# Optimization experiments

Hardware: AMD Instinct MI355X
Metric: run time of the kernel (lower is better)

The kernel has to match this reference:

```python
import jax, jax.numpy as jnp
import numpy as np

L, H, C, T, V = 6, 12, 768, 1024, 50257
HD = C // H
B = 2
EPS = 1e-5


def setup_inputs() -> dict:
    key = jax.random.key(0)
    ks = jax.random.split(key, 10)
    std = 0.02
    proj_std = 0.02 / np.sqrt(2 * L)  # specialized init for projection layers

    def n(k, shape, s=std):
        return jax.random.normal(k, shape, dtype=jnp.float32) * s

    return {
        "tokens": jax.random.randint(ks[0], (B, T), 0, V),
        "tok_emb": n(ks[1], (V, C)),
        "pos_emb": n(ks[2], (T, C)),
        # per-layer stacked params, leading dim L (scanned)
        "Wq": n(ks[3], (L, H, C, HD)),
        "Wk": n(ks[4], (L, H, C, HD)),
        "Wv": n(ks[5], (L, H, C, HD)),
        "Wo": n(ks[6], (L, C, C), proj_std),
        "bo": jnp.zeros((L, C), jnp.float32),
        "ln1_g": jnp.ones((L, C), jnp.float32),
        "ln1_b": jnp.zeros((L, C), jnp.float32),
        "ln2_g": jnp.ones((L, C), jnp.float32),
        "ln2_b": jnp.zeros((L, C), jnp.float32),
        "W1": n(ks[7], (L, C, 4 * C)),
        "b1": jnp.zeros((L, 4 * C), jnp.float32),
        "W2": n(ks[8], (L, 4 * C, C), proj_std),
        "b2": jnp.zeros((L, C), jnp.float32),
        "lnf_g": jnp.ones((C,), jnp.float32),
        "lnf_b": jnp.zeros((C,), jnp.float32),
        "head_w": n(ks[9], (C, V)),
        "head_b": jnp.zeros((V,), jnp.float32),
    }


def _ln(x, g, b):
    m = x.mean(-1, keepdims=True)
    v = ((x - m) ** 2).mean(-1, keepdims=True)
    return (x - m) * jax.lax.rsqrt(v + EPS) * g + b


def _forward(tokens, p):
    x = p["tok_emb"][tokens] + p["pos_emb"][None, : tokens.shape[1]]  # [B,T,C]
    mask = jnp.tril(jnp.ones((T, T), dtype=bool))
    scale = C ** -0.5  # NOTE: original scales by input channel C, not head_size

    def block(x, lp):
        Wq, Wk, Wv, Wo, bo, g1, b1, g2, b2, W1, bb1, W2, bb2 = lp
        # NOTE: original writes x = ln1(x); x = x + attn(x)  (residual from normed x)
        x = _ln(x, g1, b1)
        q = jnp.einsum("btc,hcd->bhtd", x, Wq)
        k = jnp.einsum("btc,hcd->bhtd", x, Wk)
        v = jnp.einsum("btc,hcd->bhtd", x, Wv)
        s = jnp.einsum("bhtd,bhsd->bhts", q, k) * scale
        s = jnp.where(mask, s, -jnp.inf)
        a = jax.nn.softmax(s, axis=-1)
        y = jnp.einsum("bhts,bhsd->bhtd", a, v)
        y = y.transpose(0, 2, 1, 3).reshape(x.shape)  # concat heads -> [B,T,C]
        x = x + y @ Wo + bo
        x = _ln(x, g2, b2)
        h = jax.nn.gelu(x @ W1 + bb1, approximate=False)  # torch GELU = exact erf
        x = x + h @ W2 + bb2
        return x, None

    lps = (p["Wq"], p["Wk"], p["Wv"], p["Wo"], p["bo"], p["ln1_g"], p["ln1_b"],
           p["ln2_g"], p["ln2_b"], p["W1"], p["b1"], p["W2"], p["b2"])
    x, _ = jax.lax.scan(block, x, lps)
    x = _ln(x, p["lnf_g"], p["lnf_b"])
    return x @ p["head_w"] + p["head_b"]  # [B,T,V]


def reference(tokens, tok_emb, pos_emb, Wq, Wk, Wv, Wo, bo, ln1_g, ln1_b,
              ln2_g, ln2_b, W1, b1, W2, b2, lnf_g, lnf_b, head_w, head_b):
    p = dict(tok_emb=tok_emb, pos_emb=pos_emb, Wq=Wq, Wk=Wk, Wv=Wv, Wo=Wo, bo=bo,
             ln1_g=ln1_g, ln1_b=ln1_b, ln2_g=ln2_g, ln2_b=ln2_b, W1=W1, b1=b1,
             W2=W2, b2=b2, lnf_g=lnf_g, lnf_b=lnf_b, head_w=head_w, head_b=head_b)
    return _forward(tokens, p)
```

## Files before the change

kernel.cpp:

```cpp
#include <hip/hip_runtime.h>
#include <hip/hip_bf16.h>
#include <stdint.h>
#include <math.h>


#define L_ 6
#define H_ 12
#define C_ 768
#define T_ 1024
#define V_ 50257
#define VP_ 50304
#define HD_ 64
#define BT_ 2048
#define F_ 3072
#define SCALE_ 0.03608439182435161f
#define NEGBIG_ -1e30f

typedef __bf16 bf;
typedef __attribute__((ext_vector_type(8))) __bf16 bf16x8;
typedef __attribute__((ext_vector_type(4))) __bf16 bf16x4;
typedef __attribute__((ext_vector_type(4))) float f32x4;

__device__ __forceinline__ void gload16(const void* g, void* l) {
  __builtin_amdgcn_global_load_lds(
      (const __attribute__((address_space(1))) unsigned int*)g,
      (__attribute__((address_space(3))) unsigned int*)l, 16, 0, 0);
}

__device__ __forceinline__ float gelu_f(float x) {
  return 0.5f * x * (1.0f + erff(x * 0.70710678118654752f));
}

__global__ __launch_bounds__(256) void embed_k(const int* __restrict__ tok,
                                               const float* __restrict__ te,
                                               const float* __restrict__ pe,
                                               float* __restrict__ x) {
  int bt = blockIdx.x;
  int c = blockIdx.y * 256 + threadIdx.x;
  int t = bt & (T_ - 1);
  int v = tok[bt];
  x[(size_t)bt * C_ + c] = te[(size_t)v * C_ + c] + pe[(size_t)t * C_ + c];
}

__global__ __launch_bounds__(256) void ln_k(const float* __restrict__ xin,
                                            float* __restrict__ xout,
                                            bf* __restrict__ xb,
                                            const float* __restrict__ g,
                                            const float* __restrict__ b) {
  int row = blockIdx.x;
  const float* xr = xin + (size_t)row * C_;
  int tid = threadIdx.x;
  float v0 = xr[tid], v1 = xr[tid + 256], v2 = xr[tid + 512];
  float s1 = v0 + v1 + v2;
  float s2 = v0 * v0 + v1 * v1 + v2 * v2;
#pragma unroll
  for (int o = 32; o > 0; o >>= 1) {
    s1 += __shfl_xor(s1, o, 64);
    s2 += __shfl_xor(s2, o, 64);
  }
  __shared__ float r1[4], r2[4];
  int w = tid >> 6, lane = tid & 63;
  if (lane == 0) { r1[w] = s1; r2[w] = s2; }
  __syncthreads();
  float S1 = r1[0] + r1[1] + r1[2] + r1[3];
  float S2 = r2[0] + r2[1] + r2[2] + r2[3];
  float mean = S1 * (1.0f / C_);
  float var = S2 * (1.0f / C_) - mean * mean;
  float rs = rsqrtf(fmaxf(var, 0.0f) + 1e-5f);
  float* xo = xout + (size_t)row * C_;
  bf* xbo = xb + (size_t)row * C_;
  float vv[3] = {v0, v1, v2};
#pragma unroll
  for (int j = 0; j < 3; ++j) {
    int c = tid + j * 256;
    float o = (vv[j] - mean) * rs * g[c] + b[c];
    xo[c] = o;
    xbo[c] = (bf)o;
  }
}

__device__ __forceinline__ void transpose_body(const float* __restrict__ src,
                                               bf* __restrict__ dst, int src_ld,
                                               int dst_ld, int k0, int n0,
                                               int nmax) {
  __shared__ __align__(16) bf tl[64][72];
  int tid = threadIdx.x;
  int r = tid >> 2;
  int cb = (tid & 3) * 16;
#pragma unroll
  for (int j4 = 0; j4 < 4; ++j4) {
    int c = cb + j4 * 4;
    int n = n0 + c;
    size_t idx = (size_t)(k0 + r) * src_ld + n;
    const float* sp = src + idx;
    if (n + 4 <= nmax && (idx & 3) == 0) {
      f32x4 v = *(const f32x4*)sp;
      tl[r][c] = (bf)v[0];
      tl[r][c + 1] = (bf)v[1];
      tl[r][c + 2] = (bf)v[2];
      tl[r][c + 3] = (bf)v[3];
    } else {
#pragma unroll
      for (int j = 0; j < 4; ++j)
        tl[r][c + j] = (n + j < nmax) ? (bf)sp[j] : (bf)0.0f;
    }
  }
  __syncthreads();
  int n = n0 + r;
  bf16x8 w0, w1;
#pragma unroll
  for (int j = 0; j < 8; ++j) {
    w0[j] = tl[cb + j][r];
    w1[j] = tl[cb + 8 + j][r];
  }
  bf* dp = dst + (size_t)n * dst_ld + k0 + cb;
  *(bf16x8*)dp = w0;
  *(bf16x8*)(dp + 8) = w1;
}

__global__ __launch_bounds__(256) void transpose_k(const float* __restrict__ src,
                                                   bf* __restrict__ dst,
                                                   int src_ld, int dst_ld,
                                                   int nmax) {
  transpose_body(src, dst, src_ld, dst_ld, blockIdx.x * 64, blockIdx.y * 64,
                 nmax);
}

__global__ __launch_bounds__(256) void trans_layer_k(
    const float* __restrict__ Wq, const float* __restrict__ Wk,
    const float* __restrict__ Wv, const float* __restrict__ Wo,
    const float* __restrict__ W1, const float* __restrict__ W2,
    bf* __restrict__ wqkvT, bf* __restrict__ woT, bf* __restrict__ w1T,
    bf* __restrict__ w2T) {
  int r = blockIdx.x;
  if (r < 432) {
    int z = r / 12, k0 = (r % 12) * 64;
    int tsel = z / H_, hh = z % H_;
    const float* W = (tsel == 0) ? Wq : (tsel == 1) ? Wk : Wv;
    transpose_body(W + (size_t)hh * C_ * HD_,
                   wqkvT + (size_t)(tsel * C_ + hh * HD_) * C_, HD_, C_, k0, 0,
                   HD_);
  } else if (r < 576) {
    r -= 432;
    transpose_body(Wo, woT, C_, C_, (r % 12) * 64, (r / 12) * 64, C_);
  } else if (r < 1152) {
    r -= 576;
    transpose_body(W1, w1T, F_, C_, (r % 12) * 64, (r / 12) * 64, F_);
  } else {
    r -= 1152;
    transpose_body(W2, w2T, C_, F_, (r % 48) * 64, (r / 48) * 64, C_);
  }
}

template <int MODE, int BM, int BN>
__global__ __launch_bounds__(256) void gemm_bt(const bf* __restrict__ A,
                                               const bf* __restrict__ Bt,
                                               const float* __restrict__ bias,
                                               float* __restrict__ xres,
                                               bf* __restrict__ o0,
                                               bf* __restrict__ o1,
                                               bf* __restrict__ o2, int K) {
  constexpr int WM = BM / 2, WN = BN / 2;
  constexpr int MI = WM / 16, NJ = WN / 16;
  __shared__ __align__(16) bf smem[(BM + BN) * 64];
  bf* aL = smem;
  bf* bL = smem + BM * 64;
  const int tid = threadIdx.x;
  const int w = tid >> 6, lane = tid & 63;
  const int wm = w >> 1, wn = w & 1;
  const int lm = lane & 15, lg = lane >> 4;

  const int lin = blockIdx.y * gridDim.x + blockIdx.x;
  const int q8 = (gridDim.x * gridDim.y) >> 3;
  const int wg = (lin & 7) * q8 + (lin >> 3);
  const int mt = gridDim.y;
  const int m0 = (wg % mt) * BM, n0 = (wg / mt) * BN;

  const int lr8 = lane >> 3;
  const int lc8s = ((lane & 7) ^ lr8) * 8;

  f32x4 acc[MI][NJ];
#pragma unroll
  for (int i = 0; i < MI; ++i)
#pragma unroll
    for (int j = 0; j < NJ; ++j) acc[i][j] = (f32x4){0.f, 0.f, 0.f, 0.f};

  const int cXor = (lm & 7) * 8;
  for (int k0 = 0; k0 < K; k0 += 64) {
#pragma unroll
    for (int c = 0; c < BM / 32; ++c) {
      int row = w * (BM / 4) + c * 8;
      gload16(A + (size_t)(m0 + row + lr8) * K + k0 + lc8s, &aL[row * 64]);
    }
#pragma unroll
    for (int c = 0; c < BN / 32; ++c) {
      int row = w * (BN / 4) + c * 8;
      gload16(Bt + (size_t)(n0 + row + lr8) * K + k0 + lc8s, &bL[row * 64]);
    }
    __syncthreads();
#pragma unroll
    for (int ks = 0; ks < 2; ++ks) {
      const int cc = (ks * 32 + lg * 8) ^ cXor;
      bf16x8 af[MI], bfv[NJ];
#pragma unroll
      for (int i = 0; i < MI; ++i)
        af[i] = *(const bf16x8*)&aL[(wm * WM + i * 16 + lm) * 64 + cc];
#pragma unroll
      for (int j = 0; j < NJ; ++j)
        bfv[j] = *(const bf16x8*)&bL[(wn * WN + j * 16 + lm) * 64 + cc];
#pragma unroll
      for (int i = 0; i < MI; ++i)
#pragma unroll
        for (int j = 0; j < NJ; ++j)
          acc[i][j] = __builtin_amdgcn_mfma_f32_16x16x32_bf16(
              af[i], bfv[j], acc[i][j], 0, 0, 0);
    }
    __syncthreads();
  }

  if constexpr (MODE == 3) {
    int ngj[NJ];
    float bv[NJ];
#pragma unroll
    for (int j = 0; j < NJ; ++j) {
      ngj[j] = n0 + wn * WN + j * 16 + lm;
      bv[j] = (ngj[j] < V_) ? bias[ngj[j]] : 0.f;
    }
#pragma unroll
    for (int i = 0; i < MI; ++i)
#pragma unroll
      for (int r = 0; r < 4; ++r) {
        int row = m0 + wm * WM + i * 16 + lg * 4 + r;
        float* orow = xres + (size_t)row * V_;
#pragma unroll
        for (int j = 0; j < NJ; ++j)
          if (ngj[j] < V_) orow[ngj[j]] = acc[i][j][r] + bv[j];
      }
    return;
  }

  if constexpr (MODE == 0) {
    const int bb = m0 >> 10;
    if (n0 >= 2 * C_) {
      bf* sv = smem;
      __syncthreads();
#pragma unroll
      for (int i = 0; i < MI; ++i)
#pragma unroll
        for (int j = 0; j < NJ; ++j) {
          int dl = wn * WN + j * 16 + lm;
#pragma unroll
          for (int r = 0; r < 4; ++r) {
            int tl = wm * WM + i * 16 + lg * 4 + r;
            sv[dl * (BM + 8) + tl] = (bf)acc[i][j][r];
          }
        }
      __syncthreads();
      int dd_l = tid >> 1, half = tid & 1;
      size_t vrow = (size_t)bb * C_ + (n0 - 2 * C_) + dd_l;
      int t_base = m0 & (T_ - 1);
#pragma unroll
      for (int s = 0; s < 4; ++s) {
        int tt = half * 32 + s * 8;
        *(bf16x8*)(o2 + vrow * T_ + t_base + tt) =
            *(const bf16x8*)&sv[dd_l * (BM + 8) + tt];
      }
      return;
    }
    bf* dst = (n0 < C_) ? o0 : o1;
    int nb = (n0 < C_) ? n0 : n0 - C_;
    size_t basej[NJ];
#pragma unroll
    for (int j = 0; j < NJ; ++j) {
      int rr = nb + wn * WN + j * 16 + lm;
      int hh = rr >> 6, dd = rr & 63;
      basej[j] = ((size_t)(bb * H_ + hh) * T_) * HD_ + dd;
    }
#pragma unroll
    for (int i = 0; i < MI; ++i)
#pragma unroll
      for (int r = 0; r < 4; ++r) {
        int tt = (m0 + wm * WM + i * 16 + lg * 4 + r) & (T_ - 1);
#pragma unroll
        for (int j = 0; j < NJ; ++j)
          dst[basej[j] + (size_t)tt * HD_] = (bf)acc[i][j][r];
      }
    return;
  }

  int ngj[NJ];
  float bv[NJ];
#pragma unroll
  for (int j = 0; j < NJ; ++j) {
    ngj[j] = n0 + wn * WN + j * 16 + lm;
    bv[j] = bias[ngj[j]];
  }
#pragma unroll
  for (int i = 0; i < MI; ++i)
#pragma unroll
    for (int r = 0; r < 4; ++r) {
      int row = m0 + wm * WM + i * 16 + lg * 4 + r;
      if constexpr (MODE == 1) {
        float* xrow = xres + (size_t)row * C_;
#pragma unroll
        for (int j = 0; j < NJ; ++j) xrow[ngj[j]] += acc[i][j][r] + bv[j];
      } else {
        bf* orow = o0 + (size_t)row * F_;
#pragma unroll
        for (int j = 0; j < NJ; ++j)
          orow[ngj[j]] = (bf)gelu_f(acc[i][j][r] + bv[j]);
      }
    }
}

__global__ __launch_bounds__(256) void attn_k(const bf* __restrict__ q,
                                              const bf* __restrict__ k,
                                              const bf* __restrict__ vt,
                                              bf* __restrict__ yb) {
  const int qb = blockIdx.x, bh = blockIdx.y;
  const int tid = threadIdx.x, w = tid >> 6, lane = tid & 63;
  const int lm = lane & 15, lg = lane >> 4;
  const int bb = bh / H_, hh = bh % H_;
  __shared__ __align__(16) bf kl[64 * 64];
  __shared__ __align__(16) bf vl[64 * 64];
  __shared__ __align__(16) bf pl[4][16 * 64];

  const int qrow = qb * 64 + w * 16 + lm;
  const bf* qbase = q + ((size_t)bh * T_ + qrow) * HD_;
  bf16x8 qf0 = *(const bf16x8*)(qbase + lg * 8);
  bf16x8 qf1 = *(const bf16x8*)(qbase + 32 + lg * 8);

  f32x4 y[4];
#pragma unroll
  for (int i = 0; i < 4; ++i) y[i] = (f32x4){0.f, 0.f, 0.f, 0.f};
  float m_run = NEGBIG_, l_run = 0.f;

  for (int kb = 0; kb <= qb; ++kb) {
#pragma unroll
    for (int c = 0; c < 2; ++c) {
      int rbase = w * 16 + c * 8;
      gload16(k + ((size_t)bh * T_ + kb * 64 + rbase + lane / 8) * HD_ +
                  (lane % 8) * 8,
              &kl[rbase * 64]);
      gload16(vt + ((size_t)bh * HD_ + rbase + lane / 8) * T_ + kb * 64 +
                  (lane % 8) * 8,
              &vl[rbase * 64]);
    }
    __syncthreads();

    f32x4 s[4];
#pragma unroll
    for (int t = 0; t < 4; ++t) {
      s[t] = (f32x4){0.f, 0.f, 0.f, 0.f};
      bf16x8 a0 = *(const bf16x8*)&kl[(t * 16 + lm) * 64 + lg * 8];
      s[t] = __builtin_amdgcn_mfma_f32_16x16x32_bf16(a0, qf0, s[t], 0, 0, 0);
      bf16x8 a1 = *(const bf16x8*)&kl[(t * 16 + lm) * 64 + 32 + lg * 8];
      s[t] = __builtin_amdgcn_mfma_f32_16x16x32_bf16(a1, qf1, s[t], 0, 0, 0);
    }

    float mx = NEGBIG_;
#pragma unroll
    for (int t = 0; t < 4; ++t)
#pragma unroll
      for (int r = 0; r < 4; ++r) {
        float v = s[t][r] * SCALE_;
        int kv = kb * 64 + t * 16 + lg * 4 + r;
        if (kb == qb && kv > qrow) v = NEGBIG_;
        s[t][r] = v;
        mx = fmaxf(mx, v);
      }
    mx = fmaxf(mx, __shfl_xor(mx, 16, 64));
    mx = fmaxf(mx, __shfl_xor(mx, 32, 64));
    float mnew = fmaxf(m_run, mx);
    float corr = __expf(m_run - mnew);
    float rs = 0.f;
#pragma unroll
    for (int t = 0; t < 4; ++t)
#pragma unroll
      for (int r = 0; r < 4; ++r) {
        float p = __expf(s[t][r] - mnew);
        s[t][r] = p;
        rs += p;
      }
    rs += __shfl_xor(rs, 16, 64);
    rs += __shfl_xor(rs, 32, 64);
    l_run = l_run * corr + rs;
    m_run = mnew;

#pragma unroll
    for (int t = 0; t < 4; ++t) {
      bf16x4 pk;
#pragma unroll
      for (int r = 0; r < 4; ++r) pk[r] = (bf)s[t][r];
      *(bf16x4*)&pl[w][lm * 64 + t * 16 + lg * 4] = pk;
    }

    float cy0 = __shfl(corr, lg * 4 + 0, 64);
    float cy1 = __shfl(corr, lg * 4 + 1, 64);
    float cy2 = __shfl(corr, lg * 4 + 2, 64);
    float cy3 = __shfl(corr, lg * 4 + 3, 64);
#pragma unroll
    for (int nt = 0; nt < 4; ++nt) {
      y[nt][0] *= cy0;
      y[nt][1] *= cy1;
      y[nt][2] *= cy2;
      y[nt][3] *= cy3;
    }

#pragma unroll
    for (int nt = 0; nt < 4; ++nt)
#pragma unroll
      for (int ks = 0; ks < 2; ++ks) {
        bf16x8 ap = *(const bf16x8*)&pl[w][lm * 64 + ks * 32 + lg * 8];
        bf16x8 bv = *(const bf16x8*)&vl[(nt * 16 + lm) * 64 + ks * 32 + lg * 8];
        y[nt] = __builtin_amdgcn_mfma_f32_16x16x32_bf16(ap, bv, y[nt], 0, 0, 0);
      }
    __syncthreads();
  }

  float ly[4];
#pragma unroll
  for (int r = 0; r < 4; ++r) ly[r] = __shfl(l_run, lg * 4 + r, 64);
#pragma unroll
  for (int nt = 0; nt < 4; ++nt) {
    int cc = hh * 64 + nt * 16 + lm;
#pragma unroll
    for (int r = 0; r < 4; ++r) {
      int qr = qb * 64 + w * 16 + lg * 4 + r;
      yb[((size_t)(bb * T_ + qr)) * C_ + cc] = (bf)(y[nt][r] / ly[r]);
    }
  }
}

extern "C" void kernel_launch(void* const* d_in, const int* in_sizes, int n_in,
                              void* d_out, int out_size, void* d_ws,
                              size_t ws_size, hipStream_t stream) {
  (void)in_sizes; (void)n_in; (void)out_size; (void)ws_size;
  const int* tokens = (const int*)d_in[0];
  const float* tok_emb = (const float*)d_in[1];
  const float* pos_emb = (const float*)d_in[2];
  const float* Wq = (const float*)d_in[3];
  const float* Wk = (const float*)d_in[4];
  const float* Wv = (const float*)d_in[5];
  const float* Wo = (const float*)d_in[6];
  const float* bo = (const float*)d_in[7];
  const float* ln1g = (const float*)d_in[8];
  const float* ln1b = (const float*)d_in[9];
  const float* ln2g = (const float*)d_in[10];
  const float* ln2b = (const float*)d_in[11];
  const float* W1 = (const float*)d_in[12];
  const float* b1 = (const float*)d_in[13];
  const float* W2 = (const float*)d_in[14];
  const float* b2 = (const float*)d_in[15];
  const float* lnfg = (const float*)d_in[16];
  const float* lnfb = (const float*)d_in[17];
  const float* headw = (const float*)d_in[18];
  const float* headb = (const float*)d_in[19];
  float* out = (float*)d_out;

  uint8_t* base = (uint8_t*)d_ws;
  size_t off = 0;
  auto alloc = [&](size_t n) -> uint8_t* {
    uint8_t* r = base + off;
    off += (n + 255) & ~(size_t)255;
    return r;
  };
  float* x = (float*)alloc((size_t)BT_ * C_ * 4);
  bf* xb = (bf*)alloc((size_t)BT_ * C_ * 2);
  bf* qq = (bf*)alloc((size_t)BT_ * C_ * 2);
  bf* kk = (bf*)alloc((size_t)BT_ * C_ * 2);
  bf* vt = (bf*)alloc((size_t)BT_ * C_ * 2);
  bf* ybuf = (bf*)alloc((size_t)BT_ * C_ * 2);
  bf* hb = (bf*)alloc((size_t)BT_ * F_ * 2);
  bf* wqkvT = (bf*)alloc((size_t)3 * C_ * C_ * 2);
  bf* woT = (bf*)alloc((size_t)C_ * C_ * 2);
  bf* w1T = (bf*)alloc((size_t)F_ * C_ * 2);
  bf* w2T = (bf*)alloc((size_t)C_ * F_ * 2);
  bf* headT = (bf*)alloc((size_t)VP_ * C_ * 2);

  dim3 blk(256);
  transpose_k<<<dim3(C_ / 64, VP_ / 64), blk, 0, stream>>>(headw, headT, V_,
                                                           C_, V_);
  embed_k<<<dim3(BT_, 3), blk, 0, stream>>>(tokens, tok_emb, pos_emb, x);

  for (int l = 0; l < L_; ++l) {
    trans_layer_k<<<1728, blk, 0, stream>>>(
        Wq + (size_t)l * H_ * C_ * HD_, Wk + (size_t)l * H_ * C_ * HD_,
        Wv + (size_t)l * H_ * C_ * HD_, Wo + (size_t)l * C_ * C_,
        W1 + (size_t)l * C_ * F_, W2 + (size_t)l * F_ * C_, wqkvT, woT, w1T,
        w2T);

    ln_k<<<BT_, blk, 0, stream>>>(x, x, xb, ln1g + l * C_, ln1b + l * C_);
    gemm_bt<0, 64, 128><<<dim3(2304 / 128, BT_ / 64), blk, 0, stream>>>(
        xb, wqkvT, nullptr, nullptr, qq, kk, vt, C_);
    attn_k<<<dim3(T_ / 64, 2 * H_), blk, 0, stream>>>(qq, kk, vt, ybuf);
    gemm_bt<1, 64, 64><<<dim3(C_ / 64, BT_ / 64), blk, 0, stream>>>(
        ybuf, woT, bo + l * C_, x, nullptr, nullptr, nullptr, C_);
    ln_k<<<BT_, blk, 0, stream>>>(x, x, xb, ln2g + l * C_, ln2b + l * C_);
    gemm_bt<2, 128, 128><<<dim3(F_ / 128, BT_ / 128), blk, 0, stream>>>(
        xb, w1T, b1 + l * F_, nullptr, hb, nullptr, nullptr, C_);
    gemm_bt<1, 64, 64><<<dim3(C_ / 64, BT_ / 64), blk, 0, stream>>>(
        hb, w2T, b2 + l * C_, x, nullptr, nullptr, nullptr, F_);
  }

  ln_k<<<BT_, blk, 0, stream>>>(x, x, xb, lnfg, lnfb);
  gemm_bt<3, 128, 128><<<dim3(VP_ / 128, BT_ / 128), blk, 0, stream>>>(
      xb, headT, headb, out, nullptr, nullptr, nullptr, C_);
}
```

Baseline: 1.374 ms.

## Double-buffer LDS tiles in GEMM and attention to overlap loads with MFMA

```diff
diff --git a/kernel.cpp b/kernel.cpp
--- a/kernel.cpp
+++ b/kernel.cpp
@@ -162,9 +162,8 @@
                                                bf* __restrict__ o2, int K) {
   constexpr int WM = BM / 2, WN = BN / 2;
   constexpr int MI = WM / 16, NJ = WN / 16;
-  __shared__ __align__(16) bf smem[(BM + BN) * 64];
-  bf* aL = smem;
-  bf* bL = smem + BM * 64;
+  constexpr int HALF = (BM + BN) * 64;
+  __shared__ __align__(16) bf smem[2 * HALF];
   const int tid = threadIdx.x;
   const int w = tid >> 6, lane = tid & 63;
   const int wm = w >> 1, wn = w & 1;
@@ -179,14 +178,9 @@
   const int lr8 = lane >> 3;
   const int lc8s = ((lane & 7) ^ lr8) * 8;
 
-  f32x4 acc[MI][NJ];
-#pragma unroll
-  for (int i = 0; i < MI; ++i)
-#pragma unroll
-    for (int j = 0; j < NJ; ++j) acc[i][j] = (f32x4){0.f, 0.f, 0.f, 0.f};
-
-  const int cXor = (lm & 7) * 8;
-  for (int k0 = 0; k0 < K; k0 += 64) {
+  auto stage = [&](int buf, int k0) {
+    bf* aL = smem + buf * HALF;
+    bf* bL = aL + BM * 64;
 #pragma unroll
     for (int c = 0; c < BM / 32; ++c) {
       int row = w * (BM / 4) + c * 8;
@@ -197,7 +191,23 @@
       int row = w * (BN / 4) + c * 8;
       gload16(Bt + (size_t)(n0 + row + lr8) * K + k0 + lc8s, &bL[row * 64]);
     }
-    __syncthreads();
+  };
+
+  f32x4 acc[MI][NJ];
+#pragma unroll
+  for (int i = 0; i < MI; ++i)
+#pragma unroll
+    for (int j = 0; j < NJ; ++j) acc[i][j] = (f32x4){0.f, 0.f, 0.f, 0.f};
+
+  const int cXor = (lm & 7) * 8;
+  const int NT = K >> 6;
+  stage(0, 0);
+  __syncthreads();
+  int cur = 0;
+  for (int t = 0; t < NT; ++t) {
+    if (t + 1 < NT) stage(cur ^ 1, (t + 1) << 6);
+    const bf* aL = smem + cur * HALF;
+    const bf* bL = aL + BM * 64;
 #pragma unroll
     for (int ks = 0; ks < 2; ++ks) {
       const int cc = (ks * 32 + lg * 8) ^ cXor;
@@ -216,6 +226,7 @@
               af[i], bfv[j], acc[i][j], 0, 0, 0);
     }
     __syncthreads();
+    cur ^= 1;
   }
 
   if constexpr (MODE == 3) {
@@ -243,7 +254,6 @@
     const int bb = m0 >> 10;
     if (n0 >= 2 * C_) {
       bf* sv = smem;
-      __syncthreads();
 #pragma unroll
       for (int i = 0; i < MI; ++i)
 #pragma unroll
@@ -321,9 +331,22 @@
   const int tid = threadIdx.x, w = tid >> 6, lane = tid & 63;
   const int lm = lane & 15, lg = lane >> 4;
   const int bb = bh / H_, hh = bh % H_;
-  __shared__ __align__(16) bf kl[64 * 64];
-  __shared__ __align__(16) bf vl[64 * 64];
+  __shared__ __align__(16) bf kl[2][64 * 64];
+  __shared__ __align__(16) bf vl[2][64 * 64];
   __shared__ __align__(16) bf pl[4][16 * 64];
+
+  auto stage = [&](int buf, int kb) {
+#pragma unroll
+    for (int c = 0; c < 2; ++c) {
+      int rbase = w * 16 + c * 8;
+      gload16(k + ((size_t)bh * T_ + kb * 64 + rbase + lane / 8) * HD_ +
+                  (lane % 8) * 8,
+              &kl[buf][rbase * 64]);
+      gload16(vt + ((size_t)bh * HD_ + rbase + lane / 8) * T_ + kb * 64 +
+                  (lane % 8) * 8,
+              &vl[buf][rbase * 64]);
+    }
+  };
 
   const int qrow = qb * 64 + w * 16 + lm;
   const bf* qbase = q + ((size_t)bh * T_ + qrow) * HD_;
@@ -335,26 +358,19 @@
   for (int i = 0; i < 4; ++i) y[i] = (f32x4){0.f, 0.f, 0.f, 0.f};
   float m_run = NEGBIG_, l_run = 0.f;
 
+  stage(0, 0);
+  __syncthreads();
+  int cur = 0;
   for (int kb = 0; kb <= qb; ++kb) {
-#pragma unroll
-    for (int c = 0; c < 2; ++c) {
-      int rbase = w * 16 + c * 8;
-      gload16(k + ((size_t)bh * T_ + kb * 64 + rbase + lane / 8) * HD_ +
-                  (lane % 8) * 8,
-              &kl[rbase * 64]);
-      gload16(vt + ((size_t)bh * HD_ + rbase + lane / 8) * T_ + kb * 64 +
-                  (lane % 8) * 8,
-              &vl[rbase * 64]);
-    }
-    __syncthreads();
+    if (kb < qb) stage(cur ^ 1, kb + 1);
 
     f32x4 s[4];
 #pragma unroll
     for (int t = 0; t < 4; ++t) {
       s[t] = (f32x4){0.f, 0.f, 0.f, 0.f};
-      bf16x8 a0 = *(const bf16x8*)&kl[(t * 16 + lm) * 64 + lg * 8];
+      bf16x8 a0 = *(const bf16x8*)&kl[cur][(t * 16 + lm) * 64 + lg * 8];
       s[t] = __builtin_amdgcn_mfma_f32_16x16x32_bf16(a0, qf0, s[t], 0, 0, 0);
-      bf16x8 a1 = *(const bf16x8*)&kl[(t * 16 + lm) * 64 + 32 + lg * 8];
+      bf16x8 a1 = *(const bf16x8*)&kl[cur][(t * 16 + lm) * 64 + 32 + lg * 8];
       s[t] = __builtin_amdgcn_mfma_f32_16x16x32_bf16(a1, qf1, s[t], 0, 0, 0);
     }
 
@@ -412,10 +428,12 @@
 #pragma unroll
       for (int ks = 0; ks < 2; ++ks) {
         bf16x8 ap = *(const bf16x8*)&pl[w][lm * 64 + ks * 32 + lg * 8];
-        bf16x8 bv = *(const bf16x8*)&vl[(nt * 16 + lm) * 64 + ks * 32 + lg * 8];
+        bf16x8 bv =
+            *(const bf16x8*)&vl[cur][(nt * 16 + lm) * 64 + ks * 32 + lg * 8];
         y[nt] = __builtin_amdgcn_mfma_f32_16x16x32_bf16(ap, bv, y[nt], 0, 0, 0);
       }
     __syncthreads();
+    cur ^= 1;
   }
 
   float ly[4];
```

Result: faster. 1.319 ms (-4.0%).
